# Optimization experiments

Hardware: AMD Instinct MI355X
Metric: run time of the kernel (lower is better)

Reference implementation:

```python
import jax, jax.numpy as jnp
import numpy as np

D_MODEL = 1024
ED = 2048          # d_inner = 2 * d_model
N = 16             # d_state
DT_RANK = 64
K = 4              # d_conv
BETA = 0.6
ALPHA = 1.0
B_SZ, L = 1, 2048


def setup_inputs() -> dict:
    key = jax.random.key(0)
    ks = jax.random.split(key, 9)
    s = 0.02
    x = jax.random.normal(ks[0], (B_SZ, L, D_MODEL), jnp.float32)
    W_in = jax.random.normal(ks[1], (2 * ED, D_MODEL), jnp.float32) * s
    conv_w = jax.random.normal(ks[2], (ED, K), jnp.float32) * s
    conv_b = jax.random.normal(ks[3], (ED,), jnp.float32) * s
    W_x = jax.random.normal(ks[4], (DT_RANK + 2 * N, ED), jnp.float32) * s
    dt_std = DT_RANK ** -0.5
    W_dt = jax.random.uniform(ks[5], (ED, DT_RANK), jnp.float32, -dt_std, dt_std)
    # dt bias init: inverse-softplus of dt in [dt_min, dt_max]
    dt = jnp.exp(jax.random.uniform(ks[6], (ED,), jnp.float32)
                 * (np.log(0.1) - np.log(0.001)) + np.log(0.001))
    dt = jnp.clip(dt, 1e-4)
    b_dt = dt + jnp.log(-jnp.expm1(-dt))
    A_log = jnp.log(jnp.tile(jnp.arange(1, N + 1, dtype=jnp.float32), (ED, 1)))
    D = jnp.ones((ED,), jnp.float32)
    W_out = jax.random.normal(ks[7], (D_MODEL, ED), jnp.float32) * s
    return {"x": x, "W_in": W_in, "conv_w": conv_w, "conv_b": conv_b,
            "W_x": W_x, "W_dt": W_dt, "b_dt": b_dt, "A_log": A_log,
            "D": D, "W_out": W_out}


def _depthwise_causal_conv(xc, conv_w, conv_b):
    # xc: (B, L, ED); torch Conv1d(groups=ED, padding=K-1)[..., :L] == causal conv
    lhs = jnp.transpose(xc, (0, 2, 1))                       # (B, ED, L)
    lhs = jnp.pad(lhs, ((0, 0), (0, 0), (K - 1, 0)))
    out = jax.lax.conv_general_dilated(lhs, conv_w[:, None, :], (1,), 'VALID',
                                       feature_group_count=ED)  # (B, ED, L)
    return jnp.transpose(out, (0, 2, 1)) + conv_b


def _ssm_momentum(xc, W_x, W_dt, b_dt, A_log, D):
    A = -jnp.exp(A_log)                                      # (ED, N)
    dBC = xc @ W_x.T                                         # (B, L, dt_rank + 2N)
    delta, Bm, Cm = jnp.split(dBC, [DT_RANK, DT_RANK + N], axis=-1)
    delta = jax.nn.softplus(delta @ W_dt.T + b_dt)           # (B, L, ED)
    deltaA = jnp.exp(delta[..., None] * A)                   # (B, L, ED, N)
    u = ALPHA * delta[..., None] * Bm[:, :, None, :] * xc[..., None]  # (B, L, ED, N)

    def step(carry, inp):
        h, v = carry
        dA_t, u_t = inp
        v = BETA * v + u_t
        h = dA_t * h + v
        return (h, v), h

    h0 = jnp.zeros((xc.shape[0], ED, N), xc.dtype)
    _, hs = jax.lax.scan(step, (h0, h0),
                         (jnp.moveaxis(deltaA, 1, 0), jnp.moveaxis(u, 1, 0)))
    y = jnp.einsum('lben,bln->ble', hs, Cm)                  # (B, L, ED)
    return y + D * xc


def reference(x, W_in, conv_w, conv_b, W_x, W_dt, b_dt, A_log, D, W_out):
    xz = x @ W_in.T                                          # (B, L, 2*ED)
    xc, z = jnp.split(xz, 2, axis=-1)
    xc = jax.nn.silu(_depthwise_causal_conv(xc, conv_w, conv_b))
    y = _ssm_momentum(xc, W_x, W_dt, b_dt, A_log, D)
    return (y * jax.nn.silu(z)) @ W_out.T                    # (B, L, d_model)
```

## Files before the change

kernel.cpp:

```cpp
#include <hip/hip_runtime.h>
#include <hip/hip_bf16.h>
#include <math.h>

#define L 2048
#define DM 1024
#define ED 2048
#define NST 16
#define DTR 64
#define BETA 0.6f
#define NCHUNK 64
#define LCH 32
#define SPLITS 16
#define SPLIT4 4

typedef __bf16 bf16_t;
typedef __bf16 bf16x8 __attribute__((ext_vector_type(8)));
typedef __bf16 bf16x4 __attribute__((ext_vector_type(4)));
typedef __bf16 bf16x2 __attribute__((ext_vector_type(2)));
typedef float  floatx4 __attribute__((ext_vector_type(4)));


__global__ void k_fill(float* __restrict__ p, float v, int n) {
    int i = blockIdx.x * 256 + threadIdx.x;
    if (i < n) p[i] = v;
}

__global__ void k_cvt_all(const float4* __restrict__ s0, bf16x4* __restrict__ d0,
                          const float4* __restrict__ s1, bf16x4* __restrict__ d1,
                          const float4* __restrict__ s2, bf16x4* __restrict__ d2,
                          const float4* __restrict__ s3, bf16x4* __restrict__ d3,
                          const float4* __restrict__ s4, bf16x4* __restrict__ d4) {
    int i = blockIdx.x * 256 + threadIdx.x;
    const float4* s; bf16x4* d; int j;
    if (i < 524288)        { s = s0; d = d0; j = i; }
    else if (i < 1572864)  { s = s1; d = d1; j = i - 524288; }
    else if (i < 1622016)  { s = s2; d = d2; j = i - 1572864; }
    else if (i < 1654784)  { s = s3; d = d3; j = i - 1622016; }
    else                   { s = s4; d = d4; j = i - 1654784; }
    float4 f = s[j];
    bf16x4 o;
    o[0] = (bf16_t)f.x; o[1] = (bf16_t)f.y; o[2] = (bf16_t)f.z; o[3] = (bf16_t)f.w;
    d[j] = o;
}

template<int EPI, bool GUARD>
__global__ __launch_bounds__(256)
void k_gemm_bt(const bf16_t* __restrict__ X, int lda,
               const bf16_t* __restrict__ W,
               float* __restrict__ C, int M, int N, int K, int ldc, int ksz,
               const float* __restrict__ bias,
               const float* __restrict__ cw, const float* __restrict__ cb) {
    __shared__ bf16_t As[128 * 32];
    __shared__ bf16_t Bs[128 * 32];
    const int tid  = threadIdx.x;
    const int bx   = blockIdx.x, by = blockIdx.y;
    const int kbase = blockIdx.z * ksz;
    const size_t zoff = (size_t)blockIdx.z * M * ldc;
    const int wave = tid >> 6, lane = tid & 63;
    const int wm   = (wave >> 1) * 64;
    const int wn   = (wave & 1) * 64;
    const int quad = lane >> 4, l16 = lane & 15;

    floatx4 acc[4][4];
#pragma unroll
    for (int i = 0; i < 4; i++)
#pragma unroll
        for (int j = 0; j < 4; j++)
            acc[i][j] = (floatx4){0.f, 0.f, 0.f, 0.f};

    for (int kt = kbase; kt < kbase + ksz; kt += 32) {
        if (GUARD) {
#pragma unroll
            for (int p = 0; p < 2; p++) {
                int e = p * 2048 + tid * 8;
                int r = e >> 5, c = e & 31;
                int t   = by * 128 + r;
                int col = kt + c;
                float accv[8];
#pragma unroll
                for (int j = 0; j < 8; j++) accv[j] = cb[col + j];
                float4 wj[8];
#pragma unroll
                for (int j = 0; j < 8; j++)
                    wj[j] = *(const float4*)(&cw[(col + j) * 4]);
#pragma unroll
                for (int k = 0; k < 4; k++) {
                    int tt = t - 3 + k;
                    if (tt >= 0) {
                        bf16x8 xv = *(const bf16x8*)(&X[(size_t)tt * lda + col]);
#pragma unroll
                        for (int j = 0; j < 8; j++)
                            accv[j] += ((const float*)&wj[j])[k] * (float)xv[j];
                    }
                }
                bf16x8 av;
#pragma unroll
                for (int j = 0; j < 8; j++) {
                    float s = accv[j] / (1.f + __expf(-accv[j]));
                    av[j] = (bf16_t)s;
                }
                *(bf16x8*)(&As[r * 32 + c]) = av;
                int brow = bx * 128 + r;
                float4 bv = make_float4(0.f, 0.f, 0.f, 0.f);
                if (brow < N) bv = *(const float4*)(&W[(size_t)brow * K + kt + c]);
                *(float4*)(&Bs[r * 32 + c]) = bv;
            }
        } else {
#pragma unroll
            for (int p = 0; p < 2; p++) {
                int e = p * 2048 + tid * 8;
                int r = e >> 5, c = e & 31;
                __builtin_amdgcn_global_load_lds(
                    (const __attribute__((address_space(1))) void*)&X[(size_t)(by * 128 + r) * lda + kt + c],
                    (__attribute__((address_space(3))) void*)&As[e], 16, 0, 0);
                __builtin_amdgcn_global_load_lds(
                    (const __attribute__((address_space(1))) void*)&W[(size_t)(bx * 128 + r) * K + kt + c],
                    (__attribute__((address_space(3))) void*)&Bs[e], 16, 0, 0);
            }
        }
        __syncthreads();

        bf16x8 af[4], bfr[4];
#pragma unroll
        for (int mt = 0; mt < 4; mt++)
            af[mt] = *(const bf16x8*)(&As[(wm + mt * 16 + l16) * 32 + quad * 8]);
#pragma unroll
        for (int nt = 0; nt < 4; nt++)
            bfr[nt] = *(const bf16x8*)(&Bs[(wn + nt * 16 + l16) * 32 + quad * 8]);
#pragma unroll
        for (int mt = 0; mt < 4; mt++)
#pragma unroll
            for (int nt = 0; nt < 4; nt++)
                acc[mt][nt] = __builtin_amdgcn_mfma_f32_16x16x32_bf16(
                    af[mt], bfr[nt], acc[mt][nt], 0, 0, 0);
        __syncthreads();
    }

#pragma unroll
    for (int mt = 0; mt < 4; mt++) {
#pragma unroll
        for (int nt = 0; nt < 4; nt++) {
            int col = bx * 128 + wn + nt * 16 + l16;
            if (!GUARD || col < N) {
#pragma unroll
                for (int r4 = 0; r4 < 4; r4++) {
                    int row = by * 128 + wm + mt * 16 + quad * 4 + r4;
                    float v = acc[mt][nt][r4];
                    size_t off = zoff + (size_t)row * ldc + col;
                    if (EPI == 0) {
                        C[off] = v;
                    } else if (EPI == 1) {
                        v += bias[col];
                        v = (v > 20.f) ? v : __logf(1.f + __expf(v));
                        ((bf16_t*)C)[off] = (bf16_t)v;
                    } else {
                        ((bf16_t*)C)[off] = (bf16_t)v;
                    }
                }
            }
        }
    }
}

__global__ void k_red4(const bf16x8* __restrict__ part, float4* __restrict__ out) {
    int i = blockIdx.x * 256 + threadIdx.x;
    const int stride = L * DM / 8;
    bf16x8 a = part[i], b = part[i + stride];
    bf16x8 c = part[i + 2 * stride], d = part[i + 3 * stride];
    float4 o0, o1;
    o0.x = (float)a[0] + (float)b[0] + (float)c[0] + (float)d[0];
    o0.y = (float)a[1] + (float)b[1] + (float)c[1] + (float)d[1];
    o0.z = (float)a[2] + (float)b[2] + (float)c[2] + (float)d[2];
    o0.w = (float)a[3] + (float)b[3] + (float)c[3] + (float)d[3];
    o1.x = (float)a[4] + (float)b[4] + (float)c[4] + (float)d[4];
    o1.y = (float)a[5] + (float)b[5] + (float)c[5] + (float)d[5];
    o1.z = (float)a[6] + (float)b[6] + (float)c[6] + (float)d[6];
    o1.w = (float)a[7] + (float)b[7] + (float)c[7] + (float)d[7];
    out[2 * i]     = o0;
    out[2 * i + 1] = o1;
}

__global__ void k_red2(const float* __restrict__ part, float* __restrict__ dBC,
                       bf16_t* __restrict__ dly) {
    int idx = blockIdx.x * 256 + threadIdx.x;
    int t = idx / 96, c = idx - t * 96;
    float s = 0.f;
#pragma unroll
    for (int sp = 0; sp < SPLITS; sp++) s += part[(size_t)sp * L * 96 + idx];
    dBC[idx] = s;
    if (c < 64) dly[t * 64 + c] = (bf16_t)s;
}


__global__ __launch_bounds__(256)
void k_scan_p1(const bf16_t* __restrict__ delta, const bf16_t* __restrict__ xz,
               const float* __restrict__ conv_w, const float* __restrict__ conv_b,
               const float* __restrict__ dBC, const float* __restrict__ A_log,
               float2* __restrict__ hv, bf16x2* __restrict__ pq) {
    const int chunk = blockIdx.x >> 3;
    const int e = (blockIdx.x & 7) * 256 + threadIdx.x;
    float A[NST];
#pragma unroll
    for (int n = 0; n < NST; n++) A[n] = -__expf(A_log[e * NST + n]);
    float h[NST], v[NST], p[NST], q[NST];
#pragma unroll
    for (int n = 0; n < NST; n++) { h[n] = 0.f; v[n] = 0.f; p[n] = 1.f; q[n] = 0.f; }
    float bp = 1.f;
    const int t0 = chunk * LCH;
    const bf16_t* xzx = xz + e;
    const float4 wv = *(const float4*)(&conv_w[e * 4]);
    const float cbv = conv_b[e];
    float x0 = (t0 >= 3) ? (float)xzx[(size_t)(t0 - 3) * 4096] : 0.f;
    float x1 = (t0 >= 2) ? (float)xzx[(size_t)(t0 - 2) * 4096] : 0.f;
    float x2 = (t0 >= 1) ? (float)xzx[(size_t)(t0 - 1) * 4096] : 0.f;
    for (int i = 0; i < LCH; i++) {
        int t = t0 + i;
        float x3 = (float)xzx[(size_t)t * 4096];
        float a4 = cbv + wv.x * x0 + wv.y * x1 + wv.z * x2 + wv.w * x3;
        float xcv = a4 / (1.f + __expf(-a4));
        x0 = x1; x1 = x2; x2 = x3;
        float d   = (float)delta[(size_t)t * ED + e];
        float du  = d * xcv;
        bp *= BETA;
        const float* Bp = &dBC[t * 96 + 64];
#pragma unroll
        for (int n = 0; n < NST; n++) {
            float a = __expf(d * A[n]);
            v[n] = BETA * v[n] + du * Bp[n];
            h[n] = a * h[n] + v[n];
            p[n] *= a;
            q[n] = a * q[n] + bp;
        }
    }
#pragma unroll
    for (int n = 0; n < NST; n++) {
        size_t idx = ((size_t)n * NCHUNK + chunk) * ED + e;
        hv[idx] = make_float2(h[n], v[n]);
        bf16x2 z; z[0] = (bf16_t)p[n]; z[1] = (bf16_t)q[n];
        pq[idx] = z;
    }
}

__global__ void k_combine(float2* __restrict__ hv, const bf16x2* __restrict__ pq) {
    int tid = blockIdx.x * 256 + threadIdx.x;
    int n = tid >> 11, e = tid & (ED - 1);
    float h = 0.f, v = 0.f;
    const float bl = 7.9586611e-8f;
#pragma unroll 4
    for (int c = 0; c < NCHUNK; c++) {
        size_t idx = ((size_t)n * NCHUNK + c) * ED + e;
        float2 f = hv[idx];
        bf16x2 z = pq[idx];
        hv[idx] = make_float2(h, v);
        float hn = (float)z[0] * h + (float)z[1] * v + f.x;
        v = bl * v + f.y;
        h = hn;
    }
}

__global__ __launch_bounds__(256)
void k_scan_p2(const bf16_t* __restrict__ delta, const bf16_t* __restrict__ xz,
               const float* __restrict__ conv_w, const float* __restrict__ conv_b,
               const float* __restrict__ dBC, const float* __restrict__ A_log,
               const float2* __restrict__ hv, const float* __restrict__ Dvec,
               bf16_t* __restrict__ g) {
    const int chunk = blockIdx.x >> 3;
    const int e = (blockIdx.x & 7) * 256 + threadIdx.x;
    float A[NST];
#pragma unroll
    for (int n = 0; n < NST; n++) A[n] = -__expf(A_log[e * NST + n]);
    float h[NST], v[NST];
#pragma unroll
    for (int n = 0; n < NST; n++) {
        float2 s = hv[((size_t)n * NCHUNK + chunk) * ED + e];
        h[n] = s.x; v[n] = s.y;
    }
    const float De = Dvec[e];
    const int t0 = chunk * LCH;
    const bf16_t* xzx = xz + e;
    const float4 wv = *(const float4*)(&conv_w[e * 4]);
    const float cbv = conv_b[e];
    float x0 = (t0 >= 3) ? (float)xzx[(size_t)(t0 - 3) * 4096] : 0.f;
    float x1 = (t0 >= 2) ? (float)xzx[(size_t)(t0 - 2) * 4096] : 0.f;
    float x2 = (t0 >= 1) ? (float)xzx[(size_t)(t0 - 1) * 4096] : 0.f;
    for (int i = 0; i < LCH; i++) {
        int t = t0 + i;
        float x3 = (float)xzx[(size_t)t * 4096];
        float a4 = cbv + wv.x * x0 + wv.y * x1 + wv.z * x2 + wv.w * x3;
        float xcv = a4 / (1.f + __expf(-a4));
        x0 = x1; x1 = x2; x2 = x3;
        float d   = (float)delta[(size_t)t * ED + e];
        float du  = d * xcv;
        const float* Bp = &dBC[t * 96 + 64];
        const float* Cp = &dBC[t * 96 + 80];
        float yacc = 0.f;
#pragma unroll
        for (int n = 0; n < NST; n++) {
            float a = __expf(d * A[n]);
            v[n] = BETA * v[n] + du * Bp[n];
            h[n] = a * h[n] + v[n];
            yacc += Cp[n] * h[n];
        }
        float z = (float)xz[(size_t)t * 4096 + ED + e];
        float sz = z / (1.f + __expf(-z));
        g[(size_t)t * ED + e] = (bf16_t)((yacc + De * xcv) * sz);
    }
}


extern "C" void kernel_launch(void* const* d_in, const int* in_sizes, int n_in,
                              void* d_out, int out_size, void* d_ws, size_t ws_size,
                              hipStream_t stream) {
    const float* x      = (const float*)d_in[0];
    const float* W_in   = (const float*)d_in[1];
    const float* conv_w = (const float*)d_in[2];
    const float* conv_b = (const float*)d_in[3];
    const float* W_x    = (const float*)d_in[4];
    const float* W_dt   = (const float*)d_in[5];
    const float* b_dt   = (const float*)d_in[6];
    const float* A_log  = (const float*)d_in[7];
    const float* Dv     = (const float*)d_in[8];
    const float* W_out  = (const float*)d_in[9];
    float* out = (float*)d_out;

    constexpr size_t OFF_XZ    = 0;
    constexpr size_t OFF_XC    = 33554432;
    constexpr size_t OFF_C     = 50331648;
    constexpr size_t OFF_DELTA = 58720256;
    constexpr size_t OFF_R1    = 75497472;
    constexpr size_t OFF_XBF   = 109051904;
    constexpr size_t OFF_DBC   = 113246208;
    constexpr size_t OFF_DLY   = 114032640;
    constexpr size_t OFF_WX    = 114294784;
    constexpr size_t OFF_WDT   = 114688000;
    constexpr size_t OFF_WOUT  = 114950144;
    constexpr size_t WS_NEED   = 119144448;

    if (ws_size < WS_NEED) {
        k_fill<<<(out_size + 255) / 256, 256, 0, stream>>>(out, 1.0e9f, out_size);
        return;
    }

    char* ws = (char*)d_ws;
    bf16_t* xz_bf = (bf16_t*)(ws + OFF_XZ);
    bf16_t* part4 = (bf16_t*)(ws + OFF_XZ);
    float2* hv    = (float2*)(ws + OFF_XC);
    bf16_t* delta_bf = (bf16_t*)(ws + OFF_DELTA);
    bf16_t* g_bf  = (bf16_t*)(ws + OFF_DELTA + 8388608);
    bf16_t* Win_bf  = (bf16_t*)(ws + OFF_R1);
    float*  part2   = (float*)(ws + OFF_R1 + 16777216);
    bf16x2* pq      = (bf16x2*)(ws + OFF_R1);
    bf16_t* x_bf  = (bf16_t*)(ws + OFF_XBF);
    float*  dBC   = (float*)(ws + OFF_DBC);
    bf16_t* dly   = (bf16_t*)(ws + OFF_DLY);
    bf16_t* Wx_bf  = (bf16_t*)(ws + OFF_WX);
    bf16_t* Wdt_bf = (bf16_t*)(ws + OFF_WDT);
    bf16_t* Wout_bf = (bf16_t*)(ws + OFF_WOUT);

    k_cvt_all<<<8512, 256, 0, stream>>>(
        (const float4*)x,     (bf16x4*)x_bf,
        (const float4*)W_in,  (bf16x4*)Win_bf,
        (const float4*)W_x,   (bf16x4*)Wx_bf,
        (const float4*)W_dt,  (bf16x4*)Wdt_bf,
        (const float4*)W_out, (bf16x4*)Wout_bf);

    {
        dim3 g(4096 / 128, L / 128, 1);
        k_gemm_bt<2, false><<<g, 256, 0, stream>>>(
            x_bf, DM, Win_bf, (float*)xz_bf, L, 4096, DM, 4096, DM,
            nullptr, nullptr, nullptr);
    }
    {
        dim3 g(1, L / 128, SPLITS);
        k_gemm_bt<0, true><<<g, 256, 0, stream>>>(
            xz_bf, 4096, Wx_bf, part2, L, 96, ED, 96, ED / SPLITS,
            nullptr, conv_w, conv_b);
    }
    k_red2<<<L * 96 / 256, 256, 0, stream>>>(part2, dBC, dly);
    {
        dim3 g(ED / 128, L / 128, 1);
        k_gemm_bt<1, false><<<g, 256, 0, stream>>>(
            dly, DTR, Wdt_bf, (float*)delta_bf, L, ED, DTR, ED, DTR,
            b_dt, nullptr, nullptr);
    }
    k_scan_p1<<<NCHUNK * 8, 256, 0, stream>>>(delta_bf, xz_bf, conv_w, conv_b,
                                              dBC, A_log, hv, pq);
    k_combine<<<ED * NST / 256, 256, 0, stream>>>(hv, pq);
    k_scan_p2<<<NCHUNK * 8, 256, 0, stream>>>(delta_bf, xz_bf, conv_w, conv_b,
                                              dBC, A_log, hv, Dv, g_bf);
    {
        dim3 g(DM / 128, L / 128, SPLIT4);
        k_gemm_bt<2, false><<<g, 256, 0, stream>>>(
            g_bf, ED, Wout_bf, (float*)part4, L, DM, ED, DM, ED / SPLIT4,
            nullptr, nullptr, nullptr);
    }
    k_red4<<<L * DM / 8 / 256, 256, 0, stream>>>((const bf16x8*)part4, (float4*)out);
}
```

Before: 251.0 us.

## Double-buffer LDS tiles in the unguarded GEMM path to overlap loads with MFMA

The non-guarded GEMM path now uses two LDS buffers per operand. It issues the global-to-LDS loads for the next K tile before running the MFMAs on the current tile, keeping one barrier per iteration instead of two. The goal is to hide global memory latency behind compute. This doubles LDS use per block, which may lower occupancy. Correctness relies on the single barrier ordering the async LDS loads, since no explicit vmcnt wait is visible.

New measurement: 244.6 us. 2.5% less time.

```diff
diff --git a/kernel.cpp b/kernel.cpp
--- a/kernel.cpp
+++ b/kernel.cpp
@@ -50,8 +50,8 @@
                float* __restrict__ C, int M, int N, int K, int ldc, int ksz,
                const float* __restrict__ bias,
                const float* __restrict__ cw, const float* __restrict__ cb) {
-    __shared__ bf16_t As[128 * 32];
-    __shared__ bf16_t Bs[128 * 32];
+    __shared__ bf16_t As[2][128 * 32];
+    __shared__ bf16_t Bs[2][128 * 32];
     const int tid  = threadIdx.x;
     const int bx   = blockIdx.x, by = blockIdx.y;
     const int kbase = blockIdx.z * ksz;
@@ -68,8 +68,44 @@
         for (int j = 0; j < 4; j++)
             acc[i][j] = (floatx4){0.f, 0.f, 0.f, 0.f};
 
-    for (int kt = kbase; kt < kbase + ksz; kt += 32) {
-        if (GUARD) {
+    auto stage = [&](int buf, int kt) {
+#pragma unroll
+        for (int p = 0; p < 2; p++) {
+            int e = p * 2048 + tid * 8;
+            int r = e >> 5, c = e & 31;
+            __builtin_amdgcn_global_load_lds(
+                (const __attribute__((address_space(1))) void*)&X[(size_t)(by * 128 + r) * lda + kt + c],
+                (__attribute__((address_space(3))) void*)&As[buf][e], 16, 0, 0);
+            __builtin_amdgcn_global_load_lds(
+                (const __attribute__((address_space(1))) void*)&W[(size_t)(bx * 128 + r) * K + kt + c],
+                (__attribute__((address_space(3))) void*)&Bs[buf][e], 16, 0, 0);
+        }
+    };
+
+    if (!GUARD) {
+        stage(0, kbase);
+        __syncthreads();
+        int cur = 0;
+        for (int kt = kbase; kt < kbase + ksz; kt += 32) {
+            if (kt + 32 < kbase + ksz) stage(cur ^ 1, kt + 32);
+            bf16x8 af[4], bfr[4];
+#pragma unroll
+            for (int mt = 0; mt < 4; mt++)
+                af[mt] = *(const bf16x8*)(&As[cur][(wm + mt * 16 + l16) * 32 + quad * 8]);
+#pragma unroll
+            for (int nt = 0; nt < 4; nt++)
+                bfr[nt] = *(const bf16x8*)(&Bs[cur][(wn + nt * 16 + l16) * 32 + quad * 8]);
+#pragma unroll
+            for (int mt = 0; mt < 4; mt++)
+#pragma unroll
+                for (int nt = 0; nt < 4; nt++)
+                    acc[mt][nt] = __builtin_amdgcn_mfma_f32_16x16x32_bf16(
+                        af[mt], bfr[nt], acc[mt][nt], 0, 0, 0);
+            __syncthreads();
+            cur ^= 1;
+        }
+    } else {
+        for (int kt = kbase; kt < kbase + ksz; kt += 32) {
 #pragma unroll
             for (int p = 0; p < 2; p++) {
                 int e = p * 2048 + tid * 8;
@@ -99,41 +135,29 @@
                     float s = accv[j] / (1.f + __expf(-accv[j]));
                     av[j] = (bf16_t)s;
                 }
-                *(bf16x8*)(&As[r * 32 + c]) = av;
+                *(bf16x8*)(&As[0][r * 32 + c]) = av;
                 int brow = bx * 128 + r;
                 float4 bv = make_float4(0.f, 0.f, 0.f, 0.f);
                 if (brow < N) bv = *(const float4*)(&W[(size_t)brow * K + kt + c]);
-                *(float4*)(&Bs[r * 32 + c]) = bv;
+                *(float4*)(&Bs[0][r * 32 + c]) = bv;
             }
-        } else {
-#pragma unroll
-            for (int p = 0; p < 2; p++) {
-                int e = p * 2048 + tid * 8;
-                int r = e >> 5, c = e & 31;
-                __builtin_amdgcn_global_load_lds(
-                    (const __attribute__((address_space(1))) void*)&X[(size_t)(by * 128 + r) * lda + kt + c],
-                    (__attribute__((address_space(3))) void*)&As[e], 16, 0, 0);
-                __builtin_amdgcn_global_load_lds(
-                    (const __attribute__((address_space(1))) void*)&W[(size_t)(bx * 128 + r) * K + kt + c],
-                    (__attribute__((address_space(3))) void*)&Bs[e], 16, 0, 0);
-            }
-        }
-        __syncthreads();
-
-        bf16x8 af[4], bfr[4];
-#pragma unroll
-        for (int mt = 0; mt < 4; mt++)
-            af[mt] = *(const bf16x8*)(&As[(wm + mt * 16 + l16) * 32 + quad * 8]);
-#pragma unroll
-        for (int nt = 0; nt < 4; nt++)
-            bfr[nt] = *(const bf16x8*)(&Bs[(wn + nt * 16 + l16) * 32 + quad * 8]);
-#pragma unroll
-        for (int mt = 0; mt < 4; mt++)
+            __syncthreads();
+
+            bf16x8 af[4], bfr[4];
+#pragma unroll
+            for (int mt = 0; mt < 4; mt++)
+                af[mt] = *(const bf16x8*)(&As[0][(wm + mt * 16 + l16) * 32 + quad * 8]);
 #pragma unroll
             for (int nt = 0; nt < 4; nt++)
-                acc[mt][nt] = __builtin_amdgcn_mfma_f32_16x16x32_bf16(
-                    af[mt], bfr[nt], acc[mt][nt], 0, 0, 0);
-        __syncthreads();
+                bfr[nt] = *(const bf16x8*)(&Bs[0][(wn + nt * 16 + l16) * 32 + quad * 8]);
+#pragma unroll
+            for (int mt = 0; mt < 4; mt++)
+#pragma unroll
+                for (int nt = 0; nt < 4; nt++)
+                    acc[mt][nt] = __builtin_amdgcn_mfma_f32_16x16x32_bf16(
+                        af[mt], bfr[nt], acc[mt][nt], 0, 0, 0);
+            __syncthreads();
+        }
     }
 
 #pragma unroll
```
